# Performance work log

Hardware: AMD Instinct MI355X
Metric: run time of the kernel (lower is better)

The kernel has to match this reference:

```python
import jax, jax.numpy as jnp
import numpy as np
import math

INPUT_WIDTH = 1024
KEY_WIDTH = 64
VALUE_WIDTH = 64
NUM_HEADS = 16
NUM_GROUPS = 4
HEADS_PER_GROUP = NUM_HEADS // NUM_GROUPS  # w = 4


def setup_inputs() -> dict:
    key = jax.random.key(0)
    k_x, k_q, k_k, k_v, k_p = jax.random.split(key, 5)
    n, s = 2, 2048
    # torch.nn.Linear weights are [out, in]; we store transposed [in, out] for x @ W.
    def lin(k, fan_in, fan_out):
        bound = 1.0 / math.sqrt(fan_in)
        return jax.random.uniform(k, (fan_in, fan_out), minval=-bound, maxval=bound, dtype=jnp.float32)
    return {
        "X": jax.random.normal(k_x, (n, s, INPUT_WIDTH), dtype=jnp.float32),
        "Wq": lin(k_q, INPUT_WIDTH, NUM_HEADS * KEY_WIDTH),
        "Wk": lin(k_k, INPUT_WIDTH, NUM_GROUPS * KEY_WIDTH),
        "Wv": lin(k_v, INPUT_WIDTH, NUM_GROUPS * VALUE_WIDTH),
        "Wpost": lin(k_p, NUM_HEADS * VALUE_WIDTH, INPUT_WIDTH),
    }


def reference(X, Wq, Wk, Wv, Wpost):
    n, s, _ = X.shape
    # Projections (no bias)
    Q = (X @ Wq).reshape(n, s, NUM_GROUPS, HEADS_PER_GROUP, KEY_WIDTH)  # [b,s,g,w,e]
    K = (X @ Wk).reshape(n, s, NUM_GROUPS, KEY_WIDTH)                   # [b,t,g,e]
    V = (X @ Wv).reshape(n, s, NUM_GROUPS, VALUE_WIDTH)                 # [b,t,g,e]
    scale = 1.0 / math.sqrt(KEY_WIDTH)
    # Grouped cross-attention: scores [b,s,t,g,w]
    raw = jnp.einsum('bsgwe,btge->bstgw', Q, K * scale)
    attn = jax.nn.softmax(raw, axis=2)  # softmax over key positions t
    A = jnp.einsum('bstgw,btge->bsgwe', attn, V).reshape(n, s, NUM_HEADS * VALUE_WIDTH)
    P = A @ Wpost
    return X + P
```

## Files before the change

### kernel.cpp

```cpp
#include <hip/hip_runtime.h>
#include <hip/hip_bf16.h>
#include <hip/hip_fp16.h>
#include <math.h>

typedef __attribute__((ext_vector_type(8))) short bfrag8;
typedef __attribute__((ext_vector_type(8))) _Float16 hfrag8;
typedef __attribute__((ext_vector_type(4))) float facc4;
typedef __attribute__((ext_vector_type(16))) float facc16;

#define MFMA16B(a, b, c) __builtin_amdgcn_mfma_f32_16x16x32_bf16((a), (b), (c), 0, 0, 0)
#define MFMA32B(a, b, c) __builtin_amdgcn_mfma_f32_32x32x16_bf16((a), (b), (c), 0, 0, 0)
#define MFMA32H(a, b, c) __builtin_amdgcn_mfma_f32_32x32x16_f16((a), (b), (c), 0, 0, 0)

__device__ __forceinline__ void gload_lds16(const void* g, void* l) {
    __builtin_amdgcn_global_load_lds(
        (const __attribute__((address_space(1))) void*)g,
        (__attribute__((address_space(3))) void*)l, 16, 0, 0);
}

__device__ __forceinline__ unsigned short f2bf(float f) {
    unsigned u = __float_as_uint(f);
    u += 0x7fffu + ((u >> 16) & 1u);
    return (unsigned short)(u >> 16);
}

__device__ __forceinline__ unsigned pk2(float a, float b) {
    auto h = __builtin_amdgcn_cvt_pkrtz(a, b);
    union { decltype(h) h; unsigned u; } c;
    c.h = h;
    return c.u;
}

__device__ __forceinline__ void do_transpose(const float* __restrict__ src,
                                             unsigned short* __restrict__ dst,
                                             int Kdim, int N, int nb, int kb,
                                             float (*tile)[33], int tid) {
    int tx = tid & 31, ty = tid >> 5;
#pragma unroll
    for (int r = ty; r < 32; r += 8)
        tile[r][tx] = src[(size_t)(kb + r) * N + nb + tx];
    __syncthreads();
#pragma unroll
    for (int r = ty; r < 32; r += 8)
        dst[(size_t)(nb + r) * Kdim + kb + tx] = f2bf(tile[tx][r]);
}

__global__ __launch_bounds__(256) void k_prep(
    const float* __restrict__ X, const float* __restrict__ Wq,
    const float* __restrict__ Wk, const float* __restrict__ Wv,
    const float* __restrict__ Wp,
    unsigned short* __restrict__ Xb, unsigned short* __restrict__ Wqkvt,
    unsigned short* __restrict__ Wpt) {
    __shared__ float tile[32][33];
    int blk = blockIdx.x, tid = threadIdx.x;
    if (blk < 4096) {
        int i = (blk * 256 + tid) * 4;
        float4 v = *reinterpret_cast<const float4*>(X + i);
        unsigned short o[4] = {f2bf(v.x), f2bf(v.y), f2bf(v.z), f2bf(v.w)};
        *reinterpret_cast<ulonglong1*>(Xb + i) = *reinterpret_cast<ulonglong1*>(o);
    } else if (blk < 5120) {
        int idx = blk - 4096;
        do_transpose(Wq, Wqkvt, 1024, 1024, (idx & 31) * 32, (idx >> 5) * 32, tile, tid);
    } else if (blk < 5376) {
        int idx = blk - 5120;
        do_transpose(Wk, Wqkvt + 1024 * 1024, 1024, 256, (idx & 7) * 32, (idx >> 3) * 32, tile, tid);
    } else if (blk < 5632) {
        int idx = blk - 5376;
        do_transpose(Wv, Wqkvt + 1280 * 1024, 1024, 256, (idx & 7) * 32, (idx >> 3) * 32, tile, tid);
    } else {
        int idx = blk - 5632;
        do_transpose(Wp, Wpt, 1024, 1024, (idx & 31) * 32, (idx >> 5) * 32, tile, tid);
    }
}

template <int EPI>
__global__ __launch_bounds__(256) void k_gemm_bt(
    const unsigned short* __restrict__ A, const unsigned short* __restrict__ Bt,
    int M, int N, int K,
    unsigned short* __restrict__ Qo, unsigned short* __restrict__ Ko,
    unsigned short* __restrict__ Vto,
    const float* __restrict__ Xres, float* __restrict__ Out) {
    __shared__ char lds[65536];
    const int tid = threadIdx.x;
    const int lane = tid & 63, wid = tid >> 6;
    const int wr = wid >> 1, wc = wid & 1;
    const int l15 = lane & 15, lhi = lane >> 4;
    const int m0 = blockIdx.y * 128, n0 = blockIdx.x * 128;
    const int nk = K >> 6;

    facc4 acc[4][4] = {};

    int segbase = wid * 4;
    int p0 = segbase * 1024 + lane * 16;

    auto STAGE = [&](int buf, int k0) {
#pragma unroll
        for (int i = 0; i < 4; ++i) {
            int p = p0 + i * 1024;
            int row = p >> 7;
            int src = (p & 127) ^ ((row & 7) << 4);
            gload_lds16(A + (size_t)(m0 + row) * K + k0 + (src >> 1),
                        lds + buf * 16384 + (segbase + i) * 1024);
            gload_lds16(Bt + (size_t)(n0 + row) * K + k0 + (src >> 1),
                        lds + 32768 + buf * 16384 + (segbase + i) * 1024);
        }
    };

    STAGE(0, 0);
    __syncthreads();

    for (int t = 0; t < nk; ++t) {
        const int cur = t & 1;
        if (t + 1 < nk) STAGE(cur ^ 1, (t + 1) * 64);
        const char* Ab = lds + cur * 16384;
        const char* Bb = lds + 32768 + cur * 16384;
#pragma unroll
        for (int kc = 0; kc < 2; ++kc) {
            bfrag8 af[4], bfv[4];
#pragma unroll
            for (int mi = 0; mi < 4; ++mi) {
                int row = wr * 64 + mi * 16 + l15;
                int off = (row * 128 + kc * 64 + lhi * 16) ^ ((row & 7) << 4);
                af[mi] = *reinterpret_cast<const bfrag8*>(Ab + off);
            }
#pragma unroll
            for (int ni = 0; ni < 4; ++ni) {
                int row = wc * 64 + ni * 16 + l15;
                int off = (row * 128 + kc * 64 + lhi * 16) ^ ((row & 7) << 4);
                bfv[ni] = *reinterpret_cast<const bfrag8*>(Bb + off);
            }
#pragma unroll
            for (int mi = 0; mi < 4; ++mi)
#pragma unroll
                for (int ni = 0; ni < 4; ++ni)
                    acc[mi][ni] = MFMA16B(af[mi], bfv[ni], acc[mi][ni]);
        }
        __syncthreads();
    }

    if (EPI == 0 && n0 >= 1280) {
        unsigned short* VT = (unsigned short*)lds;
#pragma unroll
        for (int mi = 0; mi < 4; ++mi)
#pragma unroll
            for (int ni = 0; ni < 4; ++ni) {
                int col = wc * 64 + ni * 16 + l15;
                int row0 = wr * 64 + mi * 16 + lhi * 4;
                unsigned long long u = 0;
#pragma unroll
                for (int r = 0; r < 4; ++r)
                    u |= (unsigned long long)__half_as_ushort(__float2half(acc[mi][ni][r]))
                         << (16 * r);
                *reinterpret_cast<unsigned long long*>(VT + col * 136 + row0) = u;
            }
        __syncthreads();
        int c = tid >> 1, half = tid & 1;
        int b = m0 >> 11;
        int g = ((n0 - 1280) >> 6) + (c >> 6);
        int e = c & 63;
        unsigned short* dstp = Vto + ((size_t)(b * 4 + g) * 64 + e) * 2048 + (m0 & 2047) + half * 64;
        const unsigned short* srcp = VT + c * 136 + half * 64;
#pragma unroll
        for (int j = 0; j < 8; ++j)
            *(reinterpret_cast<uint4*>(dstp) + j) = *(reinterpret_cast<const uint4*>(srcp) + j);
        return;
    }

#pragma unroll
    for (int mi = 0; mi < 4; ++mi)
#pragma unroll
        for (int ni = 0; ni < 4; ++ni)
#pragma unroll
            for (int r = 0; r < 4; ++r) {
                int grow = m0 + wr * 64 + mi * 16 + lhi * 4 + r;
                int gcol = n0 + wc * 64 + ni * 16 + l15;
                float v = acc[mi][ni][r];
                if (EPI == 0) {
                    int b = grow >> 11, t = grow & 2047;
                    if (gcol < 1024) {
                        Qo[(size_t)grow * 1024 + gcol] = f2bf(v * 0.18033688f);
                    } else {
                        int cc = gcol - 1024;
                        int g = cc >> 6, e = cc & 63;
                        Ko[(((size_t)(b * 4 + g) * 2048 + t) << 6) + e] = f2bf(v);
                    }
                } else {
                    size_t idx = (size_t)grow * 1024 + gcol;
                    Out[idx] = Xres[idx] + v;
                }
            }
}

__global__ __launch_bounds__(256, 2) void k_attn(
    const unsigned short* __restrict__ Q,
    const unsigned short* __restrict__ Kb,
    const unsigned short* __restrict__ Vt,
    unsigned short* __restrict__ Abuf) {
    __shared__ char smem[65536];

    const int tid = threadIdx.x;
    const int lane = tid & 63, wid = tid >> 6;
    const int kvh = wid >> 1, qw = wid & 1;
    const int l31 = lane & 31, hi = lane >> 5;

    int wg = blockIdx.x;
    int swz = ((wg & 7) << 6) | (wg >> 3);
    const int qt = swz & 15, head = (swz >> 4) & 15, b = swz >> 8;
    const int g = head >> 2;
    const size_t kvK = (size_t)(b * 4 + g) * 2048 * 64;
    const size_t kvV = (size_t)(b * 4 + g) * 64 * 2048;
    const int qrow0 = b * 2048 + qt * 128 + qw * 64;

    bfrag8 qf[2][4];
#pragma unroll
    for (int qs = 0; qs < 2; ++qs)
#pragma unroll
        for (int ks = 0; ks < 4; ++ks)
            qf[qs][ks] = *reinterpret_cast<const bfrag8*>(
                Q + (size_t)(qrow0 + qs * 32 + l31) * 1024 + head * 64 + ks * 16 + hi * 8);

    const unsigned short* srcK[4];
    const unsigned short* srcV[4];
#pragma unroll
    for (int j = 0; j < 4; ++j) {
        int seg = qw * 4 + j;
        int p = seg * 1024 + lane * 16;
        int row = p >> 7;
        int sb = (p & 127) ^ ((row & 7) << 4);
        srcK[j] = Kb + kvK + (size_t)(kvh * 64 + row) * 64 + (sb >> 1);
        srcV[j] = Vt + kvV + (size_t)row * 2048 + kvh * 64 + (sb >> 1);
    }
    const int lbK = kvh * 16384 + qw * 4096;
    const int lbV = 32768 + kvh * 16384 + qw * 4096;

    facc16 o[2][2] = {};
    float psA[2] = {0.f, 0.f}, psB[2] = {0.f, 0.f};

#pragma unroll
    for (int j = 0; j < 4; ++j) {
        gload_lds16(srcK[j], smem + lbK + j * 1024);
        gload_lds16(srcV[j], smem + lbV + j * 1024);
    }
    __syncthreads();

    for (int t = 0; t < 16; ++t) {
        const int cur = t & 1;
        if (t < 15) {
#pragma unroll
            for (int j = 0; j < 4; ++j) {
                gload_lds16(srcK[j] + (size_t)(t + 1) * (128 * 64),
                            smem + lbK + (cur ^ 1) * 8192 + j * 1024);
                gload_lds16(srcV[j] + (size_t)(t + 1) * 128,
                            smem + lbV + (cur ^ 1) * 8192 + j * 1024);
            }
        }
        const char* Kc = smem + kvh * 16384 + cur * 8192;
        const char* Vc = smem + 32768 + kvh * 16384 + cur * 8192;

        facc16 s[2][2] = {};
        __builtin_amdgcn_s_setprio(1);
#pragma unroll
        for (int ks = 0; ks < 4; ++ks)
#pragma unroll
            for (int nt = 0; nt < 2; ++nt) {
                int row = nt * 32 + l31;
                int off = (row * 128 + ks * 32 + hi * 16) ^ ((row & 7) << 4);
                bfrag8 kf = *reinterpret_cast<const bfrag8*>(Kc + off);
                s[0][nt] = MFMA32B(kf, qf[0][ks], s[0][nt]);
                s[1][nt] = MFMA32B(kf, qf[1][ks], s[1][nt]);
            }
        __builtin_amdgcn_s_setprio(0);

#pragma unroll
        for (int nt = 0; nt < 2; ++nt) {
#pragma unroll
            for (int qs = 0; qs < 2; ++qs)
#pragma unroll
                for (int e = 0; e < 16; e += 2) {
                    float e0 = __builtin_amdgcn_exp2f(s[qs][nt][e]);
                    float e1 = __builtin_amdgcn_exp2f(s[qs][nt][e + 1]);
                    s[qs][nt][e] = e0;
                    s[qs][nt][e + 1] = e1;
                    psA[qs] += e0;
                    psB[qs] += e1;
                }
#pragma unroll
            for (int kh = 0; kh < 2; ++kh) {
                const int ks = nt * 2 + kh;
                const int pb = kh * 2;
                hfrag8 pf[2];
#pragma unroll
                for (int qs = 0; qs < 2; ++qs) {
                    unsigned a0 = pk2(s[qs][nt][4 * pb + 0], s[qs][nt][4 * pb + 1]);
                    unsigned a1 = pk2(s[qs][nt][4 * pb + 2], s[qs][nt][4 * pb + 3]);
                    unsigned b0 = pk2(s[qs][nt][4 * pb + 4], s[qs][nt][4 * pb + 5]);
                    unsigned b1 = pk2(s[qs][nt][4 * pb + 6], s[qs][nt][4 * pb + 7]);
                    asm("v_permlane32_swap_b32 %0, %1" : "+v"(a0), "+v"(b0));
                    asm("v_permlane32_swap_b32 %0, %1" : "+v"(a1), "+v"(b1));
                    union { unsigned u[4]; hfrag8 h; } pu;
                    pu.u[0] = a0; pu.u[1] = a1; pu.u[2] = b0; pu.u[3] = b1;
                    pf[qs] = pu.h;
                }
#pragma unroll
                for (int ot = 0; ot < 2; ++ot) {
                    int row = ot * 32 + l31;
                    int off = (row * 128 + ks * 32 + hi * 16) ^ ((row & 7) << 4);
                    hfrag8 vf = *reinterpret_cast<const hfrag8*>(Vc + off);
                    o[0][ot] = MFMA32H(vf, pf[0], o[0][ot]);
                    o[1][ot] = MFMA32H(vf, pf[1], o[1][ot]);
                }
            }
        }
        __syncthreads();
    }

    float psum[2] = {psA[0] + psB[0], psA[1] + psB[1]};
    float* cm = (float*)smem;
#pragma unroll
    for (int qs = 0; qs < 2; ++qs) {
        __syncthreads();
        if (kvh == 1) {
#pragma unroll
            for (int ot = 0; ot < 2; ++ot)
#pragma unroll
                for (int r = 0; r < 16; ++r)
                    cm[qw * 4096 + (ot * 16 + r) * 64 + lane] = o[qs][ot][r];
            cm[8192 + qw * 64 + lane] = psum[qs];
        }
        __syncthreads();
        if (kvh == 0) {
#pragma unroll
            for (int ot = 0; ot < 2; ++ot)
#pragma unroll
                for (int r = 0; r < 16; ++r)
                    o[qs][ot][r] += cm[qw * 4096 + (ot * 16 + r) * 64 + lane];
            float l = psum[qs] + cm[8192 + qw * 64 + lane];
            l += __shfl_xor(l, 32, 64);
            float rl = 1.0f / l;
            int arow = qrow0 + qs * 32 + l31;
#pragma unroll
            for (int ot = 0; ot < 2; ++ot)
#pragma unroll
                for (int p = 0; p < 4; ++p) {
                    unsigned long long u = 0;
#pragma unroll
                    for (int r = 0; r < 4; ++r)
                        u |= (unsigned long long)f2bf(o[qs][ot][4 * p + r] * rl) << (16 * r);
                    *reinterpret_cast<unsigned long long*>(
                        Abuf + (size_t)arow * 1024 + head * 64 + ot * 32 + p * 8 + hi * 4) = u;
                }
        }
    }
}


extern "C" void kernel_launch(void* const* d_in, const int* in_sizes, int n_in,
                              void* d_out, int out_size, void* d_ws, size_t ws_size,
                              hipStream_t stream) {
    const float* X = (const float*)d_in[0];
    const float* Wq = (const float*)d_in[1];
    const float* Wk = (const float*)d_in[2];
    const float* Wv = (const float*)d_in[3];
    const float* Wpost = (const float*)d_in[4];
    float* Out = (float*)d_out;

    unsigned short* Xb = (unsigned short*)d_ws;
    unsigned short* Wqkvt = Xb + 4096 * 1024;
    unsigned short* Wpt = Wqkvt + 1536 * 1024;
    unsigned short* Qb = Wpt + 1024 * 1024;
    unsigned short* Kbuf = Qb + 4096 * 1024;
    unsigned short* Vtbuf = Kbuf + 8 * 2048 * 64;
    unsigned short* Abuf = Vtbuf + 8 * 2048 * 64;

    k_prep<<<6656, 256, 0, stream>>>(X, Wq, Wk, Wv, Wpost, Xb, Wqkvt, Wpt);

    k_gemm_bt<0><<<dim3(12, 32), 256, 0, stream>>>(Xb, Wqkvt, 4096, 1536, 1024,
                                                   Qb, Kbuf, Vtbuf, nullptr, nullptr);

    k_attn<<<512, 256, 0, stream>>>(Qb, Kbuf, Vtbuf, Abuf);

    k_gemm_bt<1><<<dim3(8, 32), 256, 0, stream>>>(Abuf, Wpt, 4096, 1024, 1024,
                                                  nullptr, nullptr, nullptr, X, Out);
}
```

Measured before the change: 93.24 us.

## Split attention KV range across four wave groups with 512-thread blocks

The attention kernel moves from 4 to 8 waves per block. Each query wave pair now covers a quarter of every KV tile, 32 keys per step instead of 64, so each wave's score accumulator and the per-wave K/V staging are halved, and the LDS swizzle for V is adapted to the narrower tile. The final combine now sums partial outputs and row sums from three waves in shared memory instead of one. The aim is more waves in flight to hide latency. In exchange the combine step grows and a tighter register budget under the new launch bounds risks spills.

After: 153.1 us. 64.2% more time.

```diff
diff --git a/kernel.cpp b/kernel.cpp
--- a/kernel.cpp
+++ b/kernel.cpp
@@ -191,7 +191,7 @@
             }
 }
 
-__global__ __launch_bounds__(256, 2) void k_attn(
+__global__ __launch_bounds__(512, 4) void k_attn(
     const unsigned short* __restrict__ Q,
     const unsigned short* __restrict__ Kb,
     const unsigned short* __restrict__ Vt,
@@ -200,7 +200,7 @@
 
     const int tid = threadIdx.x;
     const int lane = tid & 63, wid = tid >> 6;
-    const int kvh = wid >> 1, qw = wid & 1;
+    const int qw = wid & 1, kvh = wid >> 1;
     const int l31 = lane & 31, hi = lane >> 5;
 
     int wg = blockIdx.x;
@@ -219,27 +219,30 @@
             qf[qs][ks] = *reinterpret_cast<const bfrag8*>(
                 Q + (size_t)(qrow0 + qs * 32 + l31) * 1024 + head * 64 + ks * 16 + hi * 8);
 
-    const unsigned short* srcK[4];
-    const unsigned short* srcV[4];
-#pragma unroll
-    for (int j = 0; j < 4; ++j) {
-        int seg = qw * 4 + j;
+    const unsigned short* srcK[2];
+    const unsigned short* srcV[2];
+    int dstK[2], dstV[2];
+#pragma unroll
+    for (int j = 0; j < 2; ++j) {
+        int seg = qw * 2 + j;
         int p = seg * 1024 + lane * 16;
-        int row = p >> 7;
-        int sb = (p & 127) ^ ((row & 7) << 4);
-        srcK[j] = Kb + kvK + (size_t)(kvh * 64 + row) * 64 + (sb >> 1);
-        srcV[j] = Vt + kvV + (size_t)row * 2048 + kvh * 64 + (sb >> 1);
-    }
-    const int lbK = kvh * 16384 + qw * 4096;
-    const int lbV = 32768 + kvh * 16384 + qw * 4096;
+        int rK = p >> 7;
+        int cK = (p & 127) ^ ((rK & 7) << 4);
+        srcK[j] = Kb + kvK + (size_t)(kvh * 512 + rK) * 64 + (cK >> 1);
+        dstK[j] = kvh * 8192 + seg * 1024;
+        int rV = p >> 6;
+        int cV = (p & 63) ^ ((rV & 6) << 3);
+        srcV[j] = Vt + kvV + (size_t)rV * 2048 + kvh * 512 + (cV >> 1);
+        dstV[j] = 32768 + kvh * 8192 + seg * 1024;
+    }
 
     facc16 o[2][2] = {};
     float psA[2] = {0.f, 0.f}, psB[2] = {0.f, 0.f};
 
 #pragma unroll
-    for (int j = 0; j < 4; ++j) {
-        gload_lds16(srcK[j], smem + lbK + j * 1024);
-        gload_lds16(srcV[j], smem + lbV + j * 1024);
+    for (int j = 0; j < 2; ++j) {
+        gload_lds16(srcK[j], smem + dstK[j]);
+        gload_lds16(srcV[j], smem + dstV[j]);
     }
     __syncthreads();
 
@@ -247,68 +250,61 @@
         const int cur = t & 1;
         if (t < 15) {
 #pragma unroll
-            for (int j = 0; j < 4; ++j) {
-                gload_lds16(srcK[j] + (size_t)(t + 1) * (128 * 64),
-                            smem + lbK + (cur ^ 1) * 8192 + j * 1024);
-                gload_lds16(srcV[j] + (size_t)(t + 1) * 128,
-                            smem + lbV + (cur ^ 1) * 8192 + j * 1024);
-            }
-        }
-        const char* Kc = smem + kvh * 16384 + cur * 8192;
-        const char* Vc = smem + 32768 + kvh * 16384 + cur * 8192;
-
-        facc16 s[2][2] = {};
+            for (int j = 0; j < 2; ++j) {
+                gload_lds16(srcK[j] + (size_t)(t + 1) * (32 * 64),
+                            smem + dstK[j] + (cur ^ 1) * 4096);
+                gload_lds16(srcV[j] + (size_t)(t + 1) * 32,
+                            smem + dstV[j] + (cur ^ 1) * 4096);
+            }
+        }
+        const char* Kc = smem + kvh * 8192 + cur * 4096;
+        const char* Vc = smem + 32768 + kvh * 8192 + cur * 4096;
+
+        facc16 s[2] = {};
         __builtin_amdgcn_s_setprio(1);
 #pragma unroll
-        for (int ks = 0; ks < 4; ++ks)
-#pragma unroll
-            for (int nt = 0; nt < 2; ++nt) {
-                int row = nt * 32 + l31;
-                int off = (row * 128 + ks * 32 + hi * 16) ^ ((row & 7) << 4);
-                bfrag8 kf = *reinterpret_cast<const bfrag8*>(Kc + off);
-                s[0][nt] = MFMA32B(kf, qf[0][ks], s[0][nt]);
-                s[1][nt] = MFMA32B(kf, qf[1][ks], s[1][nt]);
-            }
+        for (int ks = 0; ks < 4; ++ks) {
+            int off = (l31 * 128 + ks * 32 + hi * 16) ^ ((l31 & 7) << 4);
+            bfrag8 kf = *reinterpret_cast<const bfrag8*>(Kc + off);
+            s[0] = MFMA32B(kf, qf[0][ks], s[0]);
+            s[1] = MFMA32B(kf, qf[1][ks], s[1]);
+        }
         __builtin_amdgcn_s_setprio(0);
 
 #pragma unroll
-        for (int nt = 0; nt < 2; ++nt) {
-#pragma unroll
-            for (int qs = 0; qs < 2; ++qs)
-#pragma unroll
-                for (int e = 0; e < 16; e += 2) {
-                    float e0 = __builtin_amdgcn_exp2f(s[qs][nt][e]);
-                    float e1 = __builtin_amdgcn_exp2f(s[qs][nt][e + 1]);
-                    s[qs][nt][e] = e0;
-                    s[qs][nt][e + 1] = e1;
-                    psA[qs] += e0;
-                    psB[qs] += e1;
-                }
-#pragma unroll
-            for (int kh = 0; kh < 2; ++kh) {
-                const int ks = nt * 2 + kh;
-                const int pb = kh * 2;
-                hfrag8 pf[2];
-#pragma unroll
-                for (int qs = 0; qs < 2; ++qs) {
-                    unsigned a0 = pk2(s[qs][nt][4 * pb + 0], s[qs][nt][4 * pb + 1]);
-                    unsigned a1 = pk2(s[qs][nt][4 * pb + 2], s[qs][nt][4 * pb + 3]);
-                    unsigned b0 = pk2(s[qs][nt][4 * pb + 4], s[qs][nt][4 * pb + 5]);
-                    unsigned b1 = pk2(s[qs][nt][4 * pb + 6], s[qs][nt][4 * pb + 7]);
-                    asm("v_permlane32_swap_b32 %0, %1" : "+v"(a0), "+v"(b0));
-                    asm("v_permlane32_swap_b32 %0, %1" : "+v"(a1), "+v"(b1));
-                    union { unsigned u[4]; hfrag8 h; } pu;
-                    pu.u[0] = a0; pu.u[1] = a1; pu.u[2] = b0; pu.u[3] = b1;
-                    pf[qs] = pu.h;
-                }
-#pragma unroll
-                for (int ot = 0; ot < 2; ++ot) {
-                    int row = ot * 32 + l31;
-                    int off = (row * 128 + ks * 32 + hi * 16) ^ ((row & 7) << 4);
-                    hfrag8 vf = *reinterpret_cast<const hfrag8*>(Vc + off);
-                    o[0][ot] = MFMA32H(vf, pf[0], o[0][ot]);
-                    o[1][ot] = MFMA32H(vf, pf[1], o[1][ot]);
-                }
+        for (int qs = 0; qs < 2; ++qs)
+#pragma unroll
+            for (int e = 0; e < 16; e += 2) {
+                float e0 = __builtin_amdgcn_exp2f(s[qs][e]);
+                float e1 = __builtin_amdgcn_exp2f(s[qs][e + 1]);
+                s[qs][e] = e0;
+                s[qs][e + 1] = e1;
+                psA[qs] += e0;
+                psB[qs] += e1;
+            }
+#pragma unroll
+        for (int kh = 0; kh < 2; ++kh) {
+            const int pb = kh * 2;
+            hfrag8 pf[2];
+#pragma unroll
+            for (int qs = 0; qs < 2; ++qs) {
+                unsigned a0 = pk2(s[qs][4 * pb + 0], s[qs][4 * pb + 1]);
+                unsigned a1 = pk2(s[qs][4 * pb + 2], s[qs][4 * pb + 3]);
+                unsigned b0 = pk2(s[qs][4 * pb + 4], s[qs][4 * pb + 5]);
+                unsigned b1 = pk2(s[qs][4 * pb + 6], s[qs][4 * pb + 7]);
+                asm("v_permlane32_swap_b32 %0, %1" : "+v"(a0), "+v"(b0));
+                asm("v_permlane32_swap_b32 %0, %1" : "+v"(a1), "+v"(b1));
+                union { unsigned u[4]; hfrag8 h; } pu;
+                pu.u[0] = a0; pu.u[1] = a1; pu.u[2] = b0; pu.u[3] = b1;
+                pf[qs] = pu.h;
+            }
+#pragma unroll
+            for (int ot = 0; ot < 2; ++ot) {
+                int row = ot * 32 + l31;
+                int off = row * 64 + ((kh * 32 + hi * 16) ^ ((row & 6) << 3));
+                hfrag8 vf = *reinterpret_cast<const hfrag8*>(Vc + off);
+                o[0][ot] = MFMA32H(vf, pf[0], o[0][ot]);
+                o[1][ot] = MFMA32H(vf, pf[1], o[1][ot]);
             }
         }
         __syncthreads();
@@ -316,26 +312,31 @@
 
     float psum[2] = {psA[0] + psB[0], psA[1] + psB[1]};
     float* cm = (float*)smem;
+    const int pbase = (qw * 3 + kvh - 1) * 2112;
 #pragma unroll
     for (int qs = 0; qs < 2; ++qs) {
         __syncthreads();
-        if (kvh == 1) {
+        if (kvh) {
 #pragma unroll
             for (int ot = 0; ot < 2; ++ot)
 #pragma unroll
                 for (int r = 0; r < 16; ++r)
-                    cm[qw * 4096 + (ot * 16 + r) * 64 + lane] = o[qs][ot][r];
-            cm[8192 + qw * 64 + lane] = psum[qs];
+                    cm[pbase + (ot * 16 + r) * 64 + lane] = o[qs][ot][r];
+            cm[pbase + 2048 + lane] = psum[qs];
         }
         __syncthreads();
         if (kvh == 0) {
 #pragma unroll
-            for (int ot = 0; ot < 2; ++ot)
-#pragma unroll
-                for (int r = 0; r < 16; ++r)
-                    o[qs][ot][r] += cm[qw * 4096 + (ot * 16 + r) * 64 + lane];
-            float l = psum[qs] + cm[8192 + qw * 64 + lane];
-            l += __shfl_xor(l, 32, 64);
+            for (int j = 0; j < 3; ++j) {
+                const int bb = (qw * 3 + j) * 2112;
+#pragma unroll
+                for (int ot = 0; ot < 2; ++ot)
+#pragma unroll
+                    for (int r = 0; r < 16; ++r)
+                        o[qs][ot][r] += cm[bb + (ot * 16 + r) * 64 + lane];
+                psum[qs] += cm[bb + 2048 + lane];
+            }
+            float l = psum[qs] + __shfl_xor(psum[qs], 32, 64);
             float rl = 1.0f / l;
             int arow = qrow0 + qs * 32 + l31;
 #pragma unroll
@@ -377,7 +378,7 @@
     k_gemm_bt<0><<<dim3(12, 32), 256, 0, stream>>>(Xb, Wqkvt, 4096, 1536, 1024,
                                                    Qb, Kbuf, Vtbuf, nullptr, nullptr);
 
-    k_attn<<<512, 256, 0, stream>>>(Qb, Kbuf, Vtbuf, Abuf);
+    k_attn<<<512, 512, 0, stream>>>(Qb, Kbuf, Vtbuf, Abuf);
 
     k_gemm_bt<1><<<dim3(8, 32), 256, 0, stream>>>(Abuf, Wpt, 4096, 1024, 1024,
                                                   nullptr, nullptr, nullptr, X, Out);
```
